# Performance work log

Hardware: AMD Instinct MI355X
Metric: run time of the kernel (lower is better)

Reference implementation:

```python
import jax, jax.numpy as jnp
import numpy as np

H, W, S, B = 256, 256, 16, 8  # dim=(H,W); S hardcoded in forward; B = 1 + events[-1,-1]
N = 4_000_000


def _shift2d(a, dy, dx):
    """Replicates F.pad(a, (pad(dx) + pad(dy)))[:H,:W] where pad(n)=(n,0) if n>=0 else (0,-n).
    Positive diff shifts content right/down and zero-fills; negative diff is a no-op
    (right/bottom padding followed by top-left crop is identity)."""
    sy = jnp.maximum(dy, 0)
    sx = jnp.maximum(dx, 0)
    a = jnp.roll(a, shift=(sy, sx), axis=(0, 1))
    row = jnp.arange(a.shape[0])[:, None]
    col = jnp.arange(a.shape[1])[None, :]
    return jnp.where((row >= sy) & (col >= sx), a, 0.0)


def setup_inputs():
    key = jax.random.key(0)
    k1, k2, k3, k4 = jax.random.split(key, 4)
    x = jax.random.randint(k1, (N,), 0, W).astype(jnp.float32)
    y = jax.random.randint(k2, (N,), 0, H).astype(jnp.float32)
    t = jax.random.uniform(k3, (N,), minval=1e-3, maxval=1.0)
    p = (jax.random.randint(k4, (N,), 0, 2) * 2 - 1).astype(jnp.float32)
    b = jnp.repeat(jnp.arange(B, dtype=jnp.float32), N // B)  # sorted so events[-1,-1]==B-1
    events = jnp.stack([x, y, t, p, b], axis=1)
    return {"events": events}


def _forward(events):
    x = events[:, 0]
    y = events[:, 1]
    t = events[:, 2]
    bi = events[:, 4].astype(jnp.int32)

    # per-batch time normalization: t /= max(t) within each sample
    t_max = jax.ops.segment_max(t, bi, num_segments=B)
    t = t / t_max[bi]

    xi = x.astype(jnp.int32)
    yi = y.astype(jnp.int32)

    # container: per-pixel event count histogram, (B,H,W)
    idx_c = xi + W * yi + W * H * bi
    container = jnp.zeros(B * H * W, jnp.int32).at[idx_c].add(1).reshape(B, H, W)

    # time_segment[e] = number of thresholds i/S (i=1..S-1) with t >= i/S
    thr = jnp.arange(1, S, dtype=t.dtype) / S
    ts = jnp.searchsorted(thr, t, side='right').astype(jnp.int32)

    # combiner accumulates the segment index itself (as in the torch code)
    idx_cb = xi + W * yi + W * H * ts + W * H * S * bi
    combiner = jnp.zeros(B * S * H * W, jnp.int32).at[idx_cb].add(ts)
    combiner = combiner.reshape(B, S, H, W).astype(jnp.float32)

    # per-(batch, segment) event counts and x/y centroids
    seg = bi * S + ts
    cnt = jax.ops.segment_sum(jnp.ones_like(t), seg, num_segments=B * S).reshape(B, S)
    xm = jax.ops.segment_sum(x, seg, num_segments=B * S).reshape(B, S) / cnt
    ym = jax.ops.segment_sum(y, seg, num_segments=B * S).reshape(B, S) / cnt

    # mean-shift alignment + accumulation of the S segment images
    combined = []
    for b_ in range(B):
        segment = combiner[b_, 0]
        x_mean = xm[b_, 0]
        y_mean = ym[b_, 0]
        pts = cnt[b_, 0]  # note: never updated in the original code
        for i in range(1, S):
            cond = cnt[b_, i] > pts
            tmp = jnp.where(cond, segment, combiner[b_, i])
            base = jnp.where(cond, combiner[b_, i], segment)
            dx = jnp.floor(jnp.where(cond, xm[b_, i] - x_mean, x_mean - xm[b_, i])).astype(jnp.int32)
            dy = jnp.floor(jnp.where(cond, ym[b_, i] - y_mean, y_mean - ym[b_, i])).astype(jnp.int32)
            x_mean = jnp.where(cond, xm[b_, i], x_mean)
            y_mean = jnp.where(cond, ym[b_, i], y_mean)
            segment = base + _shift2d(tmp, dy, dx)
        combined.append(jax.nn.relu(segment - S))
    combined_img = jnp.stack(combined)  # (B,H,W)

    # half-resolution count + mean-timestamp voxel grids
    hw4 = (H // 2) * (W // 2)
    idx_ct = xi // 2 + (W // 2) * (yi // 2) + (W * H * bi) // 4
    counter = jnp.zeros(B * hw4, jnp.int32).at[idx_ct].add(1).astype(jnp.float32)
    divider = jnp.where(counter == 0, 1.0, counter)
    timer = jnp.zeros(B * hw4, jnp.float32).at[idx_ct].add(t) / divider
    counter = counter.reshape(B, H // 2, W // 2)
    timer = timer.reshape(B, H // 2, W // 2)

    # 2x2 difference pooling of the count image
    dyv = container[:, ::2] - container[:, 1::2]
    dyv = (dyv[:, :, ::2] + dyv[:, :, 1::2]).astype(jnp.float32)
    dxv = container[:, :, ::2] - container[:, :, 1::2]
    dxv = (dxv[:, 1::2] + dxv[:, ::2]).astype(jnp.float32)

    # F.interpolate(scale_factor=0.5, mode='nearest') == ::2 subsampling for even H,W
    combined_half = combined_img[:, ::2, ::2]

    return jnp.stack([dxv, dyv, timer, counter, combined_half], axis=1)  # (B,5,H/2,W/2)


def reference(events):
    return _forward(events)
```

## Files before the change

### kernel.cpp

```cpp
#include <hip/hip_runtime.h>

#define SS 16
#define BB 8
#define CHUNKS 32

#define OFF_CNT    0
#define OFF_XS     512
#define OFF_YS     1024
#define OFF_BMAX   1536
#define OFF_P4REP  (1536 + 4096)
#define OFF_CMREP  (1536 + 4096 + 33554432)


__global__ void k_tmax(const float4* __restrict__ ev4, int nq, unsigned* __restrict__ bmax,
                       int* __restrict__ cnt, int* __restrict__ xs, int* __restrict__ ys) {
    if (blockIdx.x == 0 && threadIdx.x < BB * SS) {
        cnt[threadIdx.x] = 0; xs[threadIdx.x] = 0; ys[threadIdx.x] = 0;
    }
    int bb = blockIdx.x >> 7;
    long base = (long)bb * nq;
    unsigned m = 0;
    for (int q = (blockIdx.x & 127) * blockDim.x + threadIdx.x; q < nq; q += 128 * blockDim.x) {
        const float4* p = ev4 + (base + q) * 5;
        float4 f0 = p[0], f1 = p[1], f3 = p[3], f4 = p[4];
        unsigned t0 = __float_as_uint(f0.z), t1 = __float_as_uint(f1.w);
        unsigned t2 = __float_as_uint(f3.x), t3 = __float_as_uint(f4.y);
        unsigned a = t0 > t1 ? t0 : t1;
        unsigned b2 = t2 > t3 ? t2 : t3;
        a = a > b2 ? a : b2;
        m = m > a ? m : a;
    }
    #pragma unroll
    for (int off = 32; off; off >>= 1) {
        unsigned o = (unsigned)__shfl_xor((int)m, off, 64);
        m = m > o ? m : o;
    }
    __shared__ unsigned sm;
    if (threadIdx.x == 0) sm = 0;
    __syncthreads();
    if ((threadIdx.x & 63) == 0) atomicMax(&sm, m);
    __syncthreads();
    if (threadIdx.x == 0) bmax[blockIdx.x] = sm;
}

__global__ void __launch_bounds__(1024, 1)
k_main(const float4* __restrict__ ev4, int nq,
       const unsigned* __restrict__ bmax,
       unsigned long long* __restrict__ p4rep,
       int* __restrict__ cnt, int* __restrict__ xs, int* __restrict__ ys) {
    __shared__ unsigned long long p4s[16384];
    __shared__ unsigned long long stat[SS];
    __shared__ unsigned stmax;
    int bb = blockIdx.x >> 5;
    int ch = blockIdx.x & 31;
    if (threadIdx.x == 0) stmax = 0u;
    if (threadIdx.x < SS) stat[threadIdx.x] = 0ull;
    for (int i = threadIdx.x; i < 16384; i += 1024) p4s[i] = 0ull;
    __syncthreads();
    if (threadIdx.x < 128) atomicMax(&stmax, bmax[bb * 128 + threadIdx.x]);
    __syncthreads();
    float tm = __uint_as_float(stmax);
    long base = (long)bb * nq;
    for (int q = ch * 1024 + threadIdx.x; q < nq; q += CHUNKS * 1024) {
        const float4* p = ev4 + (base + q) * 5;
        float4 f0 = p[0], f1 = p[1], f2 = p[2], f3 = p[3], f4 = p[4];
        float X[4] = { f0.x, f1.y, f2.z, f3.w };
        float Y[4] = { f0.y, f1.z, f2.w, f4.x };
        float T[4] = { f0.z, f1.w, f3.x, f4.y };
        #pragma unroll
        for (int k = 0; k < 4; k++) {
            int xi = (int)X[k], yi = (int)Y[k];
            float tn = __fdiv_rn(T[k], tm);
            int ts = (int)(tn * 16.0f);
            if (ts > 15) ts = 15;
            unsigned qfix = __float2uint_rn(tn * 262144.0f);
            unsigned long long v = (unsigned long long)qfix
                | (1ull << 28)
                | ((unsigned long long)((xi & 1) ^ 1) << 40)
                | ((unsigned long long)((yi & 1) ^ 1) << 52);
            atomicAdd(&p4s[((yi >> 1) << 7) + (xi >> 1)], v);
            atomicAdd(&stat[ts], 1ull | ((unsigned long long)xi << 20)
                                      | ((unsigned long long)yi << 42));
        }
    }
    __syncthreads();
    unsigned long long* dst = p4rep + (long)blockIdx.x * 16384;
    for (int i = threadIdx.x; i < 16384; i += 1024) dst[i] = p4s[i];
    if (threadIdx.x < SS) {
        unsigned long long v = stat[threadIdx.x];
        if (v) {
            int g = bb * SS + threadIdx.x;
            atomicAdd(&cnt[g], (int)(v & 0xFFFFF));
            atomicAdd(&xs[g],  (int)((v >> 20) & 0x3FFFFF));
            atomicAdd(&ys[g],  (int)(v >> 42));
        }
    }
}

__global__ void __launch_bounds__(1024, 1)
k_comb(const float4* __restrict__ ev4, int nq,
       const unsigned* __restrict__ bmax,
       const int* __restrict__ cnt, const int* __restrict__ xs, const int* __restrict__ ys,
       int* __restrict__ cmrep) {
    __shared__ int combs[16384];
    __shared__ double xm[SS], ym[SS];
    __shared__ int cs[SS], ssy[SS], ssx[SS];
    __shared__ unsigned stmax;
    int bb = blockIdx.x >> 5;
    int ch = blockIdx.x & 31;
    if (threadIdx.x == 0) stmax = 0u;
    for (int i = threadIdx.x; i < 16384; i += 1024) combs[i] = 0;
    if (threadIdx.x < SS) {
        int g = bb * SS + threadIdx.x;
        int cc = cnt[g];
        cs[threadIdx.x] = cc;
        xm[threadIdx.x] = (double)xs[g] / (double)cc;
        ym[threadIdx.x] = (double)ys[g] / (double)cc;
    }
    __syncthreads();
    if (threadIdx.x < 128) atomicMax(&stmax, bmax[bb * 128 + threadIdx.x]);
    if (threadIdx.x == 0) {
        double x_mean = xm[0], y_mean = ym[0];
        int c0 = cs[0];
        int sy[SS], sx[SS];
        for (int k = 0; k < SS; k++) { sy[k] = 0; sx[k] = 0; }
        for (int k = 1; k < SS; k++) {
            bool cond = cs[k] > c0;
            double ddx = cond ? (xm[k] - x_mean) : (x_mean - xm[k]);
            double ddy = cond ? (ym[k] - y_mean) : (y_mean - ym[k]);
            int dx = (int)floor(ddx);
            int dy = (int)floor(ddy);
            int px = dx > 0 ? dx : 0;
            int py = dy > 0 ? dy : 0;
            if (cond) {
                for (int j = 0; j < k; j++) { sy[j] += py; sx[j] += px; }
                x_mean = xm[k]; y_mean = ym[k];
            } else {
                sy[k] = py; sx[k] = px;
            }
        }
        for (int k = 0; k < SS; k++) { ssy[k] = sy[k]; ssx[k] = sx[k]; }
    }
    __syncthreads();
    float tm = __uint_as_float(stmax);
    long base = (long)bb * nq;
    for (int q = ch * 1024 + threadIdx.x; q < nq; q += CHUNKS * 1024) {
        const float4* p = ev4 + (base + q) * 5;
        float4 f0 = p[0], f1 = p[1], f2 = p[2], f3 = p[3], f4 = p[4];
        float X[4] = { f0.x, f1.y, f2.z, f3.w };
        float Y[4] = { f0.y, f1.z, f2.w, f4.x };
        float T[4] = { f0.z, f1.w, f3.x, f4.y };
        #pragma unroll
        for (int k = 0; k < 4; k++) {
            int xi = (int)X[k], yi = (int)Y[k];
            float tn = __fdiv_rn(T[k], tm);
            int ts = (int)(tn * 16.0f);
            if (ts > 15) ts = 15;
            if (ts) {
                int yy = yi + ssy[ts];
                int xx = xi + ssx[ts];
                if (yy < 256 && xx < 256 && !((yy | xx) & 1))
                    atomicAdd(&combs[((yy >> 1) << 7) + (xx >> 1)], ts);
            }
        }
    }
    __syncthreads();
    int* dst = cmrep + (long)blockIdx.x * 16384;
    for (int i = threadIdx.x; i < 16384; i += 1024) dst[i] = combs[i];
}

__global__ void k_out(const unsigned long long* __restrict__ p4rep,
                      const int* __restrict__ cmrep, float* __restrict__ out) {
    int lin = blockIdx.x * blockDim.x + threadIdx.x;
    int hp = lin & 16383;
    int b  = lin >> 14;
    long rb = (long)b * CHUNKS * 16384 + hp;
    unsigned tfix = 0; int c = 0, Ex = 0, Ey = 0, cm = 0;
    #pragma unroll 8
    for (int r = 0; r < CHUNKS; r++) {
        unsigned long long v = p4rep[rb + (long)r * 16384];
        tfix += (unsigned)(v & 0xFFFFFFFull);
        c    += (int)((v >> 28) & 0xFFF);
        Ex   += (int)((v >> 40) & 0xFFF);
        Ey   += (int)((v >> 52) & 0xFFF);
        cm   += cmrep[rb + (long)r * 16384];
    }
    float tsum = (float)(double)tfix * (1.0f / 262144.0f);
    float dxv = (float)(2 * Ex - c);
    float dyv = (float)(2 * Ey - c);
    float ctr = (float)c;
    float tmr = tsum / (c == 0 ? 1.0f : ctr);
    float cmb = (float)cm - 16.0f;
    cmb = cmb < 0.0f ? 0.0f : cmb;
    int obase = (b * 5) << 14;
    out[obase              + hp] = dxv;
    out[obase +     16384  + hp] = dyv;
    out[obase + 2 * 16384  + hp] = tmr;
    out[obase + 3 * 16384  + hp] = ctr;
    out[obase + 4 * 16384  + hp] = cmb;
}

extern "C" void kernel_launch(void* const* d_in, const int* in_sizes, int n_in,
                              void* d_out, int out_size, void* d_ws, size_t ws_size,
                              hipStream_t stream) {
    const float4* ev4 = (const float4*)d_in[0];
    int n  = in_sizes[0] / 5;
    int nb = n / BB;
    int nq = nb / 4;
    char* ws = (char*)d_ws;
    int*      cnt  = (int*)     (ws + OFF_CNT);
    int*      xs   = (int*)     (ws + OFF_XS);
    int*      ys   = (int*)     (ws + OFF_YS);
    unsigned* bmax = (unsigned*)(ws + OFF_BMAX);
    unsigned long long* p4rep = (unsigned long long*)(ws + OFF_P4REP);
    int*      cmrep = (int*)    (ws + OFF_CMREP);

    hipLaunchKernelGGL(k_tmax, dim3(1024), dim3(256),  0, stream, ev4, nq, bmax,
                       cnt, xs, ys);
    hipLaunchKernelGGL(k_main, dim3(256),  dim3(1024), 0, stream, ev4, nq, bmax,
                       p4rep, cnt, xs, ys);
    hipLaunchKernelGGL(k_comb, dim3(256),  dim3(1024), 0, stream, ev4, nq, bmax,
                       cnt, xs, ys, cmrep);
    hipLaunchKernelGGL(k_out,  dim3(512),  dim3(256),  0, stream, p4rep, cmrep,
                       (float*)d_out);
}
```

Measured before the change: 160.8 us.

## Pack per-event coords and segment into compact records for combiner pass

The main pass now writes a packed 4-byte record per event (x, y, time segment) to workspace, and the combiner pass reads these instead of re-reading the 20-byte event rows and recomputing the normalised time division. It also spreads the per-segment statistics atomics over 8 slots per segment to reduce shared-memory atomic contention, summing them at the end. The cost is an extra 16 MB write in the main pass in exchange for reading far less in the combiner pass.

Measured after the change: 149.5 us. 1.08x faster.

```diff
diff --git a/kernel.cpp b/kernel.cpp
--- a/kernel.cpp
+++ b/kernel.cpp
@@ -10,6 +10,7 @@
 #define OFF_BMAX   1536
 #define OFF_P4REP  (1536 + 4096)
 #define OFF_CMREP  (1536 + 4096 + 33554432)
+#define OFF_REC    (1536 + 4096 + 33554432 + 16777216)
 
 
 __global__ void k_tmax(const float4* __restrict__ ev4, int nq, unsigned* __restrict__ bmax,
@@ -46,27 +47,29 @@
 __global__ void __launch_bounds__(1024, 1)
 k_main(const float4* __restrict__ ev4, int nq,
        const unsigned* __restrict__ bmax,
-       unsigned long long* __restrict__ p4rep,
+       unsigned long long* __restrict__ p4rep, uint4* __restrict__ rec4,
        int* __restrict__ cnt, int* __restrict__ xs, int* __restrict__ ys) {
     __shared__ unsigned long long p4s[16384];
-    __shared__ unsigned long long stat[SS];
+    __shared__ unsigned long long stat[SS * 8];
     __shared__ unsigned stmax;
     int bb = blockIdx.x >> 5;
     int ch = blockIdx.x & 31;
     if (threadIdx.x == 0) stmax = 0u;
-    if (threadIdx.x < SS) stat[threadIdx.x] = 0ull;
+    if (threadIdx.x < SS * 8) stat[threadIdx.x] = 0ull;
     for (int i = threadIdx.x; i < 16384; i += 1024) p4s[i] = 0ull;
     __syncthreads();
     if (threadIdx.x < 128) atomicMax(&stmax, bmax[bb * 128 + threadIdx.x]);
     __syncthreads();
     float tm = __uint_as_float(stmax);
     long base = (long)bb * nq;
+    int slot = threadIdx.x & 7;
     for (int q = ch * 1024 + threadIdx.x; q < nq; q += CHUNKS * 1024) {
         const float4* p = ev4 + (base + q) * 5;
         float4 f0 = p[0], f1 = p[1], f2 = p[2], f3 = p[3], f4 = p[4];
         float X[4] = { f0.x, f1.y, f2.z, f3.w };
         float Y[4] = { f0.y, f1.z, f2.w, f4.x };
         float T[4] = { f0.z, f1.w, f3.x, f4.y };
+        unsigned r[4];
         #pragma unroll
         for (int k = 0; k < 4; k++) {
             int xi = (int)X[k], yi = (int)Y[k];
@@ -79,15 +82,19 @@
                 | ((unsigned long long)((xi & 1) ^ 1) << 40)
                 | ((unsigned long long)((yi & 1) ^ 1) << 52);
             atomicAdd(&p4s[((yi >> 1) << 7) + (xi >> 1)], v);
-            atomicAdd(&stat[ts], 1ull | ((unsigned long long)xi << 20)
-                                      | ((unsigned long long)yi << 42));
-        }
+            atomicAdd(&stat[ts * 8 + slot], 1ull | ((unsigned long long)xi << 20)
+                                                 | ((unsigned long long)yi << 42));
+            r[k] = (unsigned)xi | ((unsigned)yi << 8) | ((unsigned)ts << 16);
+        }
+        rec4[base + q] = make_uint4(r[0], r[1], r[2], r[3]);
     }
     __syncthreads();
     unsigned long long* dst = p4rep + (long)blockIdx.x * 16384;
     for (int i = threadIdx.x; i < 16384; i += 1024) dst[i] = p4s[i];
     if (threadIdx.x < SS) {
-        unsigned long long v = stat[threadIdx.x];
+        unsigned long long v = 0ull;
+        #pragma unroll
+        for (int s = 0; s < 8; s++) v += stat[threadIdx.x * 8 + s];
         if (v) {
             int g = bb * SS + threadIdx.x;
             atomicAdd(&cnt[g], (int)(v & 0xFFFFF));
@@ -98,17 +105,14 @@
 }
 
 __global__ void __launch_bounds__(1024, 1)
-k_comb(const float4* __restrict__ ev4, int nq,
-       const unsigned* __restrict__ bmax,
+k_comb(const uint4* __restrict__ rec4, int nq,
        const int* __restrict__ cnt, const int* __restrict__ xs, const int* __restrict__ ys,
        int* __restrict__ cmrep) {
     __shared__ int combs[16384];
     __shared__ double xm[SS], ym[SS];
     __shared__ int cs[SS], ssy[SS], ssx[SS];
-    __shared__ unsigned stmax;
     int bb = blockIdx.x >> 5;
     int ch = blockIdx.x & 31;
-    if (threadIdx.x == 0) stmax = 0u;
     for (int i = threadIdx.x; i < 16384; i += 1024) combs[i] = 0;
     if (threadIdx.x < SS) {
         int g = bb * SS + threadIdx.x;
@@ -118,7 +122,6 @@
         ym[threadIdx.x] = (double)ys[g] / (double)cc;
     }
     __syncthreads();
-    if (threadIdx.x < 128) atomicMax(&stmax, bmax[bb * 128 + threadIdx.x]);
     if (threadIdx.x == 0) {
         double x_mean = xm[0], y_mean = ym[0];
         int c0 = cs[0];
@@ -142,23 +145,17 @@
         for (int k = 0; k < SS; k++) { ssy[k] = sy[k]; ssx[k] = sx[k]; }
     }
     __syncthreads();
-    float tm = __uint_as_float(stmax);
     long base = (long)bb * nq;
     for (int q = ch * 1024 + threadIdx.x; q < nq; q += CHUNKS * 1024) {
-        const float4* p = ev4 + (base + q) * 5;
-        float4 f0 = p[0], f1 = p[1], f2 = p[2], f3 = p[3], f4 = p[4];
-        float X[4] = { f0.x, f1.y, f2.z, f3.w };
-        float Y[4] = { f0.y, f1.z, f2.w, f4.x };
-        float T[4] = { f0.z, f1.w, f3.x, f4.y };
+        uint4 rv = rec4[base + q];
+        unsigned R[4] = { rv.x, rv.y, rv.z, rv.w };
         #pragma unroll
         for (int k = 0; k < 4; k++) {
-            int xi = (int)X[k], yi = (int)Y[k];
-            float tn = __fdiv_rn(T[k], tm);
-            int ts = (int)(tn * 16.0f);
-            if (ts > 15) ts = 15;
+            unsigned r = R[k];
+            int ts = r >> 16;
             if (ts) {
-                int yy = yi + ssy[ts];
-                int xx = xi + ssx[ts];
+                int yy = ((r >> 8) & 255) + ssy[ts];
+                int xx = (r & 255) + ssx[ts];
                 if (yy < 256 && xx < 256 && !((yy | xx) & 1))
                     atomicAdd(&combs[((yy >> 1) << 7) + (xx >> 1)], ts);
             }
@@ -214,12 +211,13 @@
     unsigned* bmax = (unsigned*)(ws + OFF_BMAX);
     unsigned long long* p4rep = (unsigned long long*)(ws + OFF_P4REP);
     int*      cmrep = (int*)    (ws + OFF_CMREP);
+    uint4*    rec4  = (uint4*)  (ws + OFF_REC);
 
     hipLaunchKernelGGL(k_tmax, dim3(1024), dim3(256),  0, stream, ev4, nq, bmax,
                        cnt, xs, ys);
     hipLaunchKernelGGL(k_main, dim3(256),  dim3(1024), 0, stream, ev4, nq, bmax,
-                       p4rep, cnt, xs, ys);
-    hipLaunchKernelGGL(k_comb, dim3(256),  dim3(1024), 0, stream, ev4, nq, bmax,
+                       p4rep, rec4, cnt, xs, ys);
+    hipLaunchKernelGGL(k_comb, dim3(256),  dim3(1024), 0, stream, rec4, nq,
                        cnt, xs, ys, cmrep);
     hipLaunchKernelGGL(k_out,  dim3(512),  dim3(256),  0, stream, p4rep, cmrep,
                        (float*)d_out);
```
